# Kernel optimization log

Measured on AMD Instinct MI355X. Metric: run time of the kernel, lower is better.

The kernel has to match this reference:

```python
import jax, jax.numpy as jnp
import numpy as np

# static config (matches init_kwargs / chosen grid)
T, H, W = 8, 32, 32          # video token grid
WT, WH, WW = 4, 8, 8         # swin window
HEADS, HD = 16, 128
DIM = HEADS * HD             # 2048
LT = 256                     # text length
EPS = 1e-6
NT, NH, NW_ = T // WT, H // WH, W // WW
NWIN = NT * NH * NW_
WLEN = WT * WH * WW


def rmsnorm(x, g):
    # x: [..., HD], g: [HD]
    var = jnp.mean(x * x, axis=-1, keepdims=True)
    return x * jax.lax.rsqrt(var + EPS) * g


def setup_inputs() -> dict:
    key = jax.random.key(0)
    ks = jax.random.split(key, 8)
    s = 0.02
    Lv = T * H * W
    return {
        'vid': jax.random.normal(ks[0], (Lv, DIM), jnp.float32),
        'txt': jax.random.normal(ks[1], (LT, DIM), jnp.float32),
        'Wqkv_v': jax.random.normal(ks[2], (DIM, 3 * DIM), jnp.float32) * s,
        'bqkv_v': jnp.zeros((3 * DIM,), jnp.float32),
        'Wqkv_t': jax.random.normal(ks[3], (DIM, 3 * DIM), jnp.float32) * s,
        'bqkv_t': jnp.zeros((3 * DIM,), jnp.float32),
        'Wo_v': jax.random.normal(ks[4], (DIM, DIM), jnp.float32) * s,
        'bo_v': jnp.zeros((DIM,), jnp.float32),
        'Wo_t': jax.random.normal(ks[5], (DIM, DIM), jnp.float32) * s,
        'bo_t': jnp.zeros((DIM,), jnp.float32),
        'gq_v': jnp.ones((HD,), jnp.float32),
        'gk_v': jnp.ones((HD,), jnp.float32),
        'gq_t': jnp.ones((HD,), jnp.float32),
        'gk_t': jnp.ones((HD,), jnp.float32),
    }


def _forward(vid, txt, Wqkv_v, bqkv_v, Wqkv_t, bqkv_t, Wo_v, bo_v, Wo_t, bo_t,
             gq_v, gk_v, gq_t, gk_t):
    # per-modality QKV projections
    vqkv = vid @ Wqkv_v + bqkv_v                      # [Lv, 3*DIM]
    tqkv = txt @ Wqkv_t + bqkv_t                      # [LT, 3*DIM]
    # swin window partition: [T,H,W,C] -> [nWin, WLEN, 3, h, d]
    x = vqkv.reshape(NT, WT, NH, WH, NW_, WW, 3 * DIM)
    x = x.transpose(0, 2, 4, 1, 3, 5, 6).reshape(NWIN, WLEN, 3, HEADS, HD)
    vq, vk, vv = x[:, :, 0], x[:, :, 1], x[:, :, 2]
    t = tqkv.reshape(LT, 3, HEADS, HD)
    tq, tk, tv = t[:, 0], t[:, 1], t[:, 2]
    # QK norm (per-head RMSNorm with affine)
    vq, vk = rmsnorm(vq, gq_v), rmsnorm(vk, gk_v)
    tq, tk = rmsnorm(tq, gq_t), rmsnorm(tk, gk_t)
    # concat full text to every window (repeat_concat_idx)
    bt = lambda a: jnp.broadcast_to(a[None], (NWIN,) + a.shape)
    q = jnp.concatenate([vq, bt(tq)], axis=1)          # [nWin, S, h, d]
    k = jnp.concatenate([vk, bt(tk)], axis=1)
    v = jnp.concatenate([vv, bt(tv)], axis=1)
    # attention within each window (flash-varlen equivalent, equal lengths)
    scale = 1.0 / np.sqrt(HD).astype(np.float32)
    scores = jnp.einsum('nqhd,nkhd->nhqk', q, k) * scale
    p = jax.nn.softmax(scores, axis=-1)
    o = jnp.einsum('nhqk,nkhd->nqhd', p, v)            # [nWin, S, h, d]
    vo = o[:, :WLEN].reshape(NWIN, WLEN, DIM)
    to = o[:, WLEN:].mean(axis=0).reshape(LT, DIM)     # un-repeat text: mean over windows
    # window reverse -> flat [Lv, DIM]
    vo = vo.reshape(NT, NH, NW_, WT, WH, WW, DIM)
    vo = vo.transpose(0, 3, 1, 4, 2, 5, 6).reshape(T * H * W, DIM)
    return (vo @ Wo_v + bo_v, to @ Wo_t + bo_t)


def reference(vid, txt, Wqkv_v, bqkv_v, Wqkv_t, bqkv_t, Wo_v, bo_v, Wo_t, bo_t,
              gq_v, gk_v, gq_t, gk_t):
    return _forward(vid, txt, Wqkv_v, bqkv_v, Wqkv_t, bqkv_t, Wo_v, bo_v,
                    Wo_t, bo_t, gq_v, gk_v, gq_t, gk_t)
```

## Files before the change

kernel.cpp:

```cpp
#include <hip/hip_runtime.h>

typedef unsigned short u16;
typedef unsigned int   u32;
typedef __attribute__((ext_vector_type(8))) short short8;
typedef __attribute__((ext_vector_type(4))) float f32x4;

__device__ __forceinline__ u16 f2bf(float f) {
  union { float f; u32 u; } v; v.f = f;
  u32 r = v.u + 0x7fffu + ((v.u >> 16) & 1u);
  return (u16)(r >> 16);
}
__device__ __forceinline__ float bf2f(u32 bits) {
  union { u32 u; float f; } v; v.u = bits << 16; return v.f;
}
__device__ __forceinline__ void gl_lds16(const u16* g, u16* l) {
  __builtin_amdgcn_global_load_lds(
      (const __attribute__((address_space(1))) void*)g,
      (__attribute__((address_space(3))) void*)l, 16, 0, 0);
}

static constexpr int DIM  = 2048;
static constexpr int NQKV = 6144;

__global__ __launch_bounds__(256) void conv_f32_bf16(const float* __restrict__ in,
                                                     u16* __restrict__ out, int n4) {
  int id = blockIdx.x * 256 + threadIdx.x;
  if (id >= n4) return;
  float4 v = ((const float4*)in)[id];
  u32 lo = (u32)f2bf(v.x) | ((u32)f2bf(v.y) << 16);
  u32 hi = (u32)f2bf(v.z) | ((u32)f2bf(v.w) << 16);
  ((uint2*)out)[id] = make_uint2(lo, hi);
}

__global__ void tconv_kernel(const float* __restrict__ W, u16* __restrict__ Wt, int K, int N) {
  __shared__ float t[32][33];
  int tx = threadIdx.x, ty = threadIdx.y;
  int n0 = blockIdx.x * 32, k0 = blockIdx.y * 32;
  #pragma unroll
  for (int i = 0; i < 4; ++i)
    t[ty + i*8][tx] = W[(size_t)(k0 + ty + i*8) * N + n0 + tx];
  __syncthreads();
  #pragma unroll
  for (int i = 0; i < 4; ++i)
    Wt[(size_t)(n0 + ty + i*8) * K + k0 + tx] = f2bf(t[tx][ty + i*8]);
}

__global__ __launch_bounds__(256) void rms_kernel(u16* __restrict__ x,
                                                  const float* __restrict__ g, int nrows) {
  int w = threadIdx.x >> 6, lane = threadIdx.x & 63;
  int rid = blockIdx.x * 4 + w;
  if (rid >= nrows) return;
  u32* row = (u32*)x + (size_t)rid * 64;
  u32 u = row[lane];
  float f0 = bf2f(u & 0xffffu), f1 = bf2f(u >> 16);
  float s = f0*f0 + f1*f1;
  #pragma unroll
  for (int off = 1; off <= 32; off <<= 1) s += __shfl_xor(s, off);
  float r = rsqrtf(s * (1.0f/128.0f) + 1e-6f);
  float g0 = g[lane*2], g1 = g[lane*2+1];
  row[lane] = (u32)f2bf(f0*r*g0) | ((u32)f2bf(f1*r*g1) << 16);
}

__global__ __launch_bounds__(256)
void vtrans_kernel(const u16* __restrict__ src, u16* __restrict__ dst) {
  __shared__ u16 t[64][130];
  int nh = blockIdx.x, k0 = blockIdx.y * 64;
  const u16* s = src + ((size_t)nh*256 + k0)*128;
  u16* d = dst + (size_t)nh*128*256 + k0;
  int tid = threadIdx.x;
  #pragma unroll
  for (int it = 0; it < 4; ++it) {
    int c = tid + it*256;
    int row = c >> 4, ch = c & 15;
    short8 v = *(const short8*)(s + row*128 + ch*8);
    u32* dst32 = (u32*)&t[row][ch*8];
    const u32* v32 = (const u32*)&v;
    dst32[0] = v32[0]; dst32[1] = v32[1]; dst32[2] = v32[2]; dst32[3] = v32[3];
  }
  __syncthreads();
  #pragma unroll
  for (int it = 0; it < 4; ++it) {
    int c = tid + it*256;
    int dr = c >> 3, kg = c & 7;
    short8 v;
    #pragma unroll
    for (int j = 0; j < 8; ++j) v[j] = (short)t[kg*8+j][dr];
    *(short8*)(d + (size_t)dr*256 + kg*8) = v;
  }
}

template<int EPI>
__global__ __launch_bounds__(512, 2)
void gemm256(const u16* __restrict__ A, const u16* __restrict__ Bt,
             const float* __restrict__ bias,
             u16* __restrict__ o0, u16* __restrict__ o1, u16* __restrict__ o2,
             float* __restrict__ of, int ldo, int M, int N, int K)
{
  __shared__ __align__(16) u16 As[4][256*32];
  __shared__ __align__(16) u16 Bs[4][256*32];
  const int NT = K >> 5;
  int tid = threadIdx.x, lane = tid & 63, w = tid >> 6;
  int l15 = lane & 15, l4 = lane >> 4;
  int wm = w >> 2, wn = w & 3;

  int nbx = gridDim.x;
  int nwg = nbx * gridDim.y;
  int bid = blockIdx.y * nbx + blockIdx.x;
  int cpx = nwg >> 3;
  int swz = (bid & 7) * cpx + (bid >> 3);
  int n0 = (swz % nbx) * 256, m0 = (swz / nbx) * 256;

  int srow = tid >> 2, skc = (tid & 3) ^ ((tid >> 3) & 3);
  const u16* aS = A  + (size_t)(m0 + srow) * K + skc * 8;
  const u16* bS = Bt + (size_t)(n0 + srow) * K + skc * 8;
  const size_t halfStride = 128 * (size_t)K;
  const int ldsBase = w * 512;

  #define STAGE_A(slot, tt, half) \
    gl_lds16(aS + (size_t)(tt)*32 + (half)*halfStride, &As[slot][(half)*4096 + ldsBase])
  #define STAGE_B(slot, tt, half) \
    gl_lds16(bS + (size_t)(tt)*32 + (half)*halfStride, &Bs[slot][(half)*4096 + ldsBase])

  #pragma unroll
  for (int pt = 0; pt < 3; ++pt) {
    STAGE_A(pt, pt, 0); STAGE_A(pt, pt, 1);
    STAGE_B(pt, pt, 0); STAGE_B(pt, pt, 1);
  }

  f32x4 acc[8][4] = {};

  for (int t = 0; t < NT; ++t) {
    if (t < NT - 2)       asm volatile("s_waitcnt vmcnt(8)" ::: "memory");
    else if (t == NT - 2) asm volatile("s_waitcnt vmcnt(4)" ::: "memory");
    else                  asm volatile("s_waitcnt vmcnt(0)" ::: "memory");
    __builtin_amdgcn_s_barrier();
    asm volatile("" ::: "memory");

    const u16* ab = As[t & 3];
    const u16* bb = Bs[t & 3];
    bool st = (t + 3 < NT);
    int slot = (t + 3) & 3;

    short8 bf_[4];
    #pragma unroll
    for (int j = 0; j < 4; ++j) {
      int rb = wn*64 + j*16 + l15;
      bf_[j] = *(const short8*)((const char*)bb + rb*64 + ((l4 ^ ((rb>>1)&3))*16));
    }

    short8 af[4];
    #pragma unroll
    for (int i = 0; i < 4; ++i) {
      int ra = wm*128 + i*16 + l15;
      af[i] = *(const short8*)((const char*)ab + ra*64 + ((l4 ^ ((ra>>1)&3))*16));
    }
    if (st) { STAGE_A(slot, t+3, 0); STAGE_A(slot, t+3, 1); }
    __builtin_amdgcn_s_setprio(1);
    #pragma unroll
    for (int i = 0; i < 4; ++i)
      #pragma unroll
      for (int j = 0; j < 4; ++j)
        acc[i][j] = __builtin_amdgcn_mfma_f32_16x16x32_bf16(af[i], bf_[j], acc[i][j], 0, 0, 0);
    __builtin_amdgcn_s_setprio(0);

    #pragma unroll
    for (int i = 0; i < 4; ++i) {
      int ra = wm*128 + 64 + i*16 + l15;
      af[i] = *(const short8*)((const char*)ab + ra*64 + ((l4 ^ ((ra>>1)&3))*16));
    }
    if (st) { STAGE_B(slot, t+3, 0); STAGE_B(slot, t+3, 1); }
    __builtin_amdgcn_s_setprio(1);
    #pragma unroll
    for (int i = 0; i < 4; ++i)
      #pragma unroll
      for (int j = 0; j < 4; ++j)
        acc[4+i][j] = __builtin_amdgcn_mfma_f32_16x16x32_bf16(af[i], bf_[j], acc[4+i][j], 0, 0, 0);
    __builtin_amdgcn_s_setprio(0);
  }
  #undef STAGE_A
  #undef STAGE_B

  #pragma unroll
  for (int i = 0; i < 8; ++i)
    #pragma unroll
    for (int j = 0; j < 4; ++j)
      #pragma unroll
      for (int r = 0; r < 4; ++r) {
        int m = m0 + wm*128 + i*16 + l4*4 + r;
        int n = n0 + wn*64  + j*16 + l15;
        float v = acc[i][j][r] + bias[n];
        if (EPI == 0) {
          int which = n >> 11, head = (n >> 7) & 15, d = n & 127;
          int t = m >> 10, hh = (m >> 5) & 31, ww = m & 31;
          int win = ((t>>2)<<4) + ((hh>>3)<<2) + (ww>>3);
          int p   = ((t&3)<<6) + ((hh&7)<<3) + (ww&7);
          u16* dst = which == 0 ? o0 : (which == 1 ? o1 : o2);
          dst[((size_t)(win*16 + head)*256 + p)*128 + d] = f2bf(v);
        } else {
          of[(size_t)m * ldo + n] = v;
        }
      }
}

template<int EPI>
__global__ __launch_bounds__(256)
void gemm128(const u16* __restrict__ A, const u16* __restrict__ Bt,
             const float* __restrict__ bias,
             u16* __restrict__ o0, u16* __restrict__ o1, u16* __restrict__ o2,
             float* __restrict__ of, int ldo, int M, int N, int K)
{
  __shared__ __align__(16) u16 As[128*32];
  __shared__ __align__(16) u16 Bs[128*32];
  int tid = threadIdx.x, lane = tid & 63, w = tid >> 6;
  int l15 = lane & 15, l4 = lane >> 4;
  int m0 = blockIdx.y * 128, n0 = blockIdx.x * 128;
  int wr = (w >> 1) * 64, wc = (w & 1) * 64;
  f32x4 acc[4][4] = {};

  int o0b = (w    )*1024 + lane*16;
  int o1b = (w + 4)*1024 + lane*16;
  int r0 = o0b >> 6, c0 = ((o0b >> 4) & 3) ^ ((r0 >> 1) & 3);
  int r1 = o1b >> 6, c1 = ((o1b >> 4) & 3) ^ ((r1 >> 1) & 3);
  const u16* a0 = A  + (size_t)(m0 + r0)*K + c0*8;
  const u16* a1 = A  + (size_t)(m0 + r1)*K + c1*8;
  const u16* b0 = Bt + (size_t)(n0 + r0)*K + c0*8;
  const u16* b1 = Bt + (size_t)(n0 + r1)*K + c1*8;
  u16* dA0 = As + (w    )*512;
  u16* dA1 = As + (w + 4)*512;
  u16* dB0 = Bs + (w    )*512;
  u16* dB1 = Bs + (w + 4)*512;

  for (int k0 = 0; k0 < K; k0 += 32) {
    gl_lds16(a0 + k0, dA0);
    gl_lds16(a1 + k0, dA1);
    gl_lds16(b0 + k0, dB0);
    gl_lds16(b1 + k0, dB1);
    __syncthreads();
    short8 af[4], bfr[4];
    #pragma unroll
    for (int t = 0; t < 4; ++t) {
      int ra = wr + t*16 + l15;
      af[t]  = *(const short8*)((const char*)As + ra*64 + ((l4 ^ ((ra>>1)&3))*16));
      int rb = wc + t*16 + l15;
      bfr[t] = *(const short8*)((const char*)Bs + rb*64 + ((l4 ^ ((rb>>1)&3))*16));
    }
    #pragma unroll
    for (int i = 0; i < 4; ++i)
      #pragma unroll
      for (int j = 0; j < 4; ++j)
        acc[i][j] = __builtin_amdgcn_mfma_f32_16x16x32_bf16(af[i], bfr[j], acc[i][j], 0, 0, 0);
    __syncthreads();
  }

  #pragma unroll
  for (int i = 0; i < 4; ++i)
    #pragma unroll
    for (int j = 0; j < 4; ++j)
      #pragma unroll
      for (int r = 0; r < 4; ++r) {
        int m = m0 + wr + i*16 + l4*4 + r;
        int n = n0 + wc + j*16 + l15;
        float v = acc[i][j][r] + bias[n];
        if (EPI == 1) {
          int which = n >> 11, head = (n >> 7) & 15, d = n & 127;
          u16* dst = which == 0 ? o0 : (which == 1 ? o1 : o2);
          dst[((size_t)head*256 + m)*128 + d] = f2bf(v);
        } else {
          of[(size_t)m * ldo + n] = v;
        }
      }
}

__global__ __launch_bounds__(512)
void attn_kernel(const u16* __restrict__ vq, const u16* __restrict__ vk, const u16* __restrict__ vv,
                 const u16* __restrict__ tq, const u16* __restrict__ tk, const u16* __restrict__ tv,
                 const float* __restrict__ gq_v, const float* __restrict__ gq_t,
                 u16* __restrict__ vo, float* __restrict__ to_acc)
{
  __shared__ __align__(16) u16 Ks[64*128];
  __shared__ __align__(16) u16 Vt[128*64];
  __shared__ __align__(16) u16 Ps[8][16*80];
  int tid = threadIdx.x, lane = tid & 63, w = tid >> 6;
  int l15 = lane & 15, l4 = lane >> 4;
  int nh_ = blockIdx.x;
  int h = nh_ & 15;
  int n = nh_ >> 4;
  int qt = blockIdx.y * 128 + w * 16;

  const u16* Qb; const float* gq;
  if (qt < 256) { Qb = vq + ((size_t)nh_*256 + qt)*128; gq = gq_v; }
  else          { Qb = tq + ((size_t)h  *256 + (qt-256))*128; gq = gq_t; }
  short8 qf[4];
  float qv[4][8];
  float ss = 0.f;
  #pragma unroll
  for (int dt = 0; dt < 4; ++dt) {
    qf[dt] = *(const short8*)(Qb + l15*128 + l4*8 + dt*32);
    #pragma unroll
    for (int j = 0; j < 8; ++j) {
      float f = bf2f((u16)qf[dt][j]);
      qv[dt][j] = f; ss += f*f;
    }
  }
  ss += __shfl_xor(ss, 16); ss += __shfl_xor(ss, 32);
  float rr = rsqrtf(ss * (1.0f/128.0f) + 1e-6f);
  #pragma unroll
  for (int dt = 0; dt < 4; ++dt) {
    float4 g0 = *(const float4*)(gq + l4*8 + dt*32);
    float4 g1 = *(const float4*)(gq + l4*8 + dt*32 + 4);
    qf[dt][0] = (short)f2bf(qv[dt][0]*rr*g0.x); qf[dt][1] = (short)f2bf(qv[dt][1]*rr*g0.y);
    qf[dt][2] = (short)f2bf(qv[dt][2]*rr*g0.z); qf[dt][3] = (short)f2bf(qv[dt][3]*rr*g0.w);
    qf[dt][4] = (short)f2bf(qv[dt][4]*rr*g1.x); qf[dt][5] = (short)f2bf(qv[dt][5]*rr*g1.y);
    qf[dt][6] = (short)f2bf(qv[dt][6]*rr*g1.z); qf[dt][7] = (short)f2bf(qv[dt][7]*rr*g1.w);
  }

  int oK0 = w*1024 + lane*16, oK1 = oK0 + 8192;
  int kr0 = oK0 >> 8, kc0 = ((oK0 >> 4) & 15) ^ (kr0 & 7);
  int kr1 = oK1 >> 8, kc1 = ((oK1 >> 4) & 15) ^ (kr1 & 7);
  int vd0 = oK0 >> 7, vc0 = ((oK0 >> 4) & 7) ^ (vd0 & 7);
  int vd1 = oK1 >> 7, vc1 = ((oK1 >> 4) & 7) ^ (vd1 & 7);
  u16* KD0 = Ks + (w*1024)/2;  u16* KD1 = Ks + (w*1024 + 8192)/2;
  u16* VD0 = Vt + (w*1024)/2;  u16* VD1 = Vt + (w*1024 + 8192)/2;

  f32x4 o_[8] = {};
  float m_run[4] = {-1e30f,-1e30f,-1e30f,-1e30f};
  float l_run[4] = {0.f,0.f,0.f,0.f};
  const float scale = 0.08838834764831845f;

  for (int c = 0; c < 8; ++c) {
    int kb = c * 64;
    const u16* Kc; const u16* Vb; int vkb;
    if (kb < 256) { Kc = vk + ((size_t)nh_*256 + kb)*128; Vb = vv + (size_t)nh_*128*256; vkb = kb; }
    else          { Kc = tk + ((size_t)h  *256 + (kb-256))*128; Vb = tv + (size_t)h*128*256; vkb = kb - 256; }
    gl_lds16(Kc + kr0*128 + kc0*8, KD0);
    gl_lds16(Kc + kr1*128 + kc1*8, KD1);
    gl_lds16(Vb + (size_t)vd0*256 + vkb + vc0*8, VD0);
    gl_lds16(Vb + (size_t)vd1*256 + vkb + vc1*8, VD1);
    __syncthreads();

    f32x4 s4[4];
    #pragma unroll
    for (int kt = 0; kt < 4; ++kt) {
      f32x4 sa = {0.f,0.f,0.f,0.f};
      int key = kt*16 + l15;
      #pragma unroll
      for (int dt = 0; dt < 4; ++dt) {
        int c16b = l4 + dt*4;
        short8 kf = *(const short8*)((const char*)Ks + key*256 + (((c16b ^ (key&7)))*16));
        sa = __builtin_amdgcn_mfma_f32_16x16x32_bf16(qf[dt], kf, sa, 0, 0, 0);
      }
      s4[kt] = sa;
    }

    float f_[4];
    #pragma unroll
    for (int r = 0; r < 4; ++r) {
      float mx = fmaxf(fmaxf(s4[0][r], s4[1][r]), fmaxf(s4[2][r], s4[3][r])) * scale;
      #pragma unroll
      for (int off = 1; off <= 8; off <<= 1) mx = fmaxf(mx, __shfl_xor(mx, off));
      float nm = fmaxf(m_run[r], mx);
      f_[r] = __expf(m_run[r] - nm);
      m_run[r] = nm;
    }
    float p[4][4];
    #pragma unroll
    for (int kt = 0; kt < 4; ++kt)
      #pragma unroll
      for (int r = 0; r < 4; ++r)
        p[kt][r] = __expf(s4[kt][r]*scale - m_run[r]);
    #pragma unroll
    for (int r = 0; r < 4; ++r) {
      float sum = p[0][r] + p[1][r] + p[2][r] + p[3][r];
      #pragma unroll
      for (int off = 1; off <= 8; off <<= 1) sum += __shfl_xor(sum, off);
      l_run[r] = l_run[r]*f_[r] + sum;
    }
    #pragma unroll
    for (int dt = 0; dt < 8; ++dt) {
      f32x4 t = o_[dt];
      t[0]*=f_[0]; t[1]*=f_[1]; t[2]*=f_[2]; t[3]*=f_[3];
      o_[dt] = t;
    }

    u16* pb = Ps[w];
    #pragma unroll
    for (int kt = 0; kt < 4; ++kt)
      #pragma unroll
      for (int r = 0; r < 4; ++r)
        pb[(l4*4 + r)*80 + kt*16 + l15] = f2bf(p[kt][r]);
    __syncthreads();
    #pragma unroll
    for (int ks = 0; ks < 2; ++ks) {
      short8 pa = *(const short8*)((const char*)pb + l15*160 + ks*64 + l4*16);
      #pragma unroll
      for (int dt = 0; dt < 8; ++dt) {
        int d = dt*16 + l15;
        short8 vf = *(const short8*)((const char*)Vt + d*128 + (((ks*4 + l4) ^ (d&7))<<4));
        o_[dt] = __builtin_amdgcn_mfma_f32_16x16x32_bf16(pa, vf, o_[dt], 0, 0, 0);
      }
    }
    __syncthreads();
  }

  float inv[4];
  #pragma unroll
  for (int r = 0; r < 4; ++r) inv[r] = 1.0f / l_run[r];
  int nt = n >> 4, nh2 = (n >> 2) & 3, nw = n & 3;
  #pragma unroll
  for (int dt = 0; dt < 8; ++dt) {
    int d = dt*16 + l15;
    int col = h*128 + d;
    #pragma unroll
    for (int r = 0; r < 4; ++r) {
      float val = o_[dt][r] * inv[r];
      int q = qt + l4*4 + r;
      if (q < 256) {
        int wt = q >> 6, wh = (q >> 3) & 7, ww = q & 7;
        int rg = ((nt*4 + wt)*32 + (nh2*8 + wh))*32 + (nw*8 + ww);
        vo[(size_t)rg*2048 + col] = f2bf(val);
      } else {
        atomicAdd(to_acc + (size_t)(q - 256)*2048 + col, val * (1.0f/32.0f));
      }
    }
  }
}

extern "C" void kernel_launch(void* const* d_in, const int* in_sizes, int n_in,
                              void* d_out, int out_size, void* d_ws, size_t ws_size,
                              hipStream_t stream) {
  const float* vid    = (const float*)d_in[0];
  const float* txt    = (const float*)d_in[1];
  const float* Wqkv_v = (const float*)d_in[2];
  const float* bqkv_v = (const float*)d_in[3];
  const float* Wqkv_t = (const float*)d_in[4];
  const float* bqkv_t = (const float*)d_in[5];
  const float* Wo_v   = (const float*)d_in[6];
  const float* bo_v   = (const float*)d_in[7];
  const float* Wo_t   = (const float*)d_in[8];
  const float* bo_t   = (const float*)d_in[9];
  const float* gq_v   = (const float*)d_in[10];
  const float* gk_v   = (const float*)d_in[11];
  const float* gq_t   = (const float*)d_in[12];
  const float* gk_t   = (const float*)d_in[13];
  float* out = (float*)d_out;

  char* p = (char*)d_ws;
  u16* vid_bf   = (u16*)p;  p += 8192ull*2048*2;
  u16* txt_bf   = (u16*)p;  p += 256ull*2048*2;
  u16* Wqkv_v_t = (u16*)p;  p += 6144ull*2048*2;
  u16* Wqkv_t_t = (u16*)p;  p += 6144ull*2048*2;
  u16* Wo_v_t   = (u16*)p;  p += 2048ull*2048*2;
  u16* Wo_t_t   = (u16*)p;  p += 2048ull*2048*2;
  u16* vq_w     = (u16*)p;  p += 32ull*16*256*128*2;
  u16* vk_w     = (u16*)p;  p += 32ull*16*256*128*2;
  u16* vv_w     = (u16*)p;  p += 32ull*16*256*128*2;
  u16* tq_w     = (u16*)p;  p += 16ull*256*128*2;
  u16* tk_w     = (u16*)p;  p += 16ull*256*128*2;
  u16* tv_w     = (u16*)p;  p += 16ull*256*128*2;
  u16* vo_pre   = (u16*)p;  p += 8192ull*2048*2;
  float* to_pre = (float*)p; p += 256ull*2048*4;
  u16* to_bf    = (u16*)p;  p += 256ull*2048*2;
  u16* vvT = vid_bf;
  u16* tvT = vid_bf + 512ull*128*256;

  hipMemsetAsync(to_pre, 0, 256ull*2048*4, stream);

  conv_f32_bf16<<<dim3(16384), dim3(256), 0, stream>>>(vid, vid_bf, 8192*2048/4);
  conv_f32_bf16<<<dim3(512),   dim3(256), 0, stream>>>(txt, txt_bf, 256*2048/4);
  tconv_kernel<<<dim3(192,64), dim3(32,8), 0, stream>>>(Wqkv_v, Wqkv_v_t, 2048, 6144);
  tconv_kernel<<<dim3(192,64), dim3(32,8), 0, stream>>>(Wqkv_t, Wqkv_t_t, 2048, 6144);
  tconv_kernel<<<dim3(64,64),  dim3(32,8), 0, stream>>>(Wo_v,   Wo_v_t,   2048, 2048);
  tconv_kernel<<<dim3(64,64),  dim3(32,8), 0, stream>>>(Wo_t,   Wo_t_t,   2048, 2048);

  gemm256<0><<<dim3(24,32), dim3(512), 0, stream>>>(vid_bf, Wqkv_v_t, bqkv_v,
      vq_w, vk_w, vv_w, nullptr, 0, 8192, NQKV, DIM);
  gemm128<1><<<dim3(48,2),  dim3(256), 0, stream>>>(txt_bf, Wqkv_t_t, bqkv_t,
      tq_w, tk_w, tv_w, nullptr, 0, 256, NQKV, DIM);

  vtrans_kernel<<<dim3(512,4), dim3(256), 0, stream>>>(vv_w, vvT);
  vtrans_kernel<<<dim3(16,4),  dim3(256), 0, stream>>>(tv_w, tvT);

  rms_kernel<<<dim3(32768), dim3(256), 0, stream>>>(vk_w, gk_v, 32*16*256);
  rms_kernel<<<dim3(1024),  dim3(256), 0, stream>>>(tk_w, gk_t, 16*256);

  attn_kernel<<<dim3(512,4), dim3(512), 0, stream>>>(vq_w, vk_w, vvT, tq_w, tk_w, tvT,
                                                     gq_v, gq_t, vo_pre, to_pre);

  conv_f32_bf16<<<dim3(512), dim3(256), 0, stream>>>(to_pre, to_bf, 256*2048/4);

  gemm256<2><<<dim3(8,32), dim3(512), 0, stream>>>(vo_pre, Wo_v_t, bo_v,
      nullptr, nullptr, nullptr, out, 2048, 8192, 2048, 2048);
  gemm128<2><<<dim3(16,2), dim3(256), 0, stream>>>(to_bf, Wo_t_t, bo_t,
      nullptr, nullptr, nullptr, out + 16777216, 2048, 256, 2048, 2048);
}
```

Before: 641.8 us.

## Double-buffer K/V in attention, process 32 queries per wave, remap grid

The attention kernel now has each wave handle two 16-row query tiles, so one block covers 256 queries and the grid halves to 1024 blocks. The intent is to reuse each K/V tile loaded into LDS across twice as many queries. K/V tiles are double-buffered so the next chunk's global-to-LDS load overlaps the current chunk's compute, which also removes one barrier per iteration. It adds s_setprio around the MFMA sections and swizzles the block index so blocks sharing an XCD are grouped. The cost is twice the LDS for K/V plus more registers for two accumulator sets, which may lower occupancy.

```diff
diff --git a/kernel.cpp b/kernel.cpp
--- a/kernel.cpp
+++ b/kernel.cpp
@@ -277,41 +277,52 @@
                  const float* __restrict__ gq_v, const float* __restrict__ gq_t,
                  u16* __restrict__ vo, float* __restrict__ to_acc)
 {
-  __shared__ __align__(16) u16 Ks[64*128];
-  __shared__ __align__(16) u16 Vt[128*64];
-  __shared__ __align__(16) u16 Ps[8][16*80];
+  __shared__ __align__(16) u16 Ks[2*64*128];
+  __shared__ __align__(16) u16 Vt[2*128*64];
+  __shared__ __align__(16) u16 Ps[8][32*88];
   int tid = threadIdx.x, lane = tid & 63, w = tid >> 6;
   int l15 = lane & 15, l4 = lane >> 4;
-  int nh_ = blockIdx.x;
+  int bid = blockIdx.x;
+  int logical = (bid & 7) * 128 + (bid >> 3);
+  int nh_ = logical >> 1, y = logical & 1;
   int h = nh_ & 15;
   int n = nh_ >> 4;
-  int qt = blockIdx.y * 128 + w * 16;
 
   const u16* Qb; const float* gq;
-  if (qt < 256) { Qb = vq + ((size_t)nh_*256 + qt)*128; gq = gq_v; }
-  else          { Qb = tq + ((size_t)h  *256 + (qt-256))*128; gq = gq_t; }
-  short8 qf[4];
-  float qv[4][8];
-  float ss = 0.f;
-  #pragma unroll
-  for (int dt = 0; dt < 4; ++dt) {
-    qf[dt] = *(const short8*)(Qb + l15*128 + l4*8 + dt*32);
-    #pragma unroll
-    for (int j = 0; j < 8; ++j) {
-      float f = bf2f((u16)qf[dt][j]);
-      qv[dt][j] = f; ss += f*f;
-    }
-  }
-  ss += __shfl_xor(ss, 16); ss += __shfl_xor(ss, 32);
-  float rr = rsqrtf(ss * (1.0f/128.0f) + 1e-6f);
+  if (y == 0) { Qb = vq + ((size_t)nh_*256 + w*32)*128; gq = gq_v; }
+  else        { Qb = tq + ((size_t)h  *256 + w*32)*128; gq = gq_t; }
+  float g0v[4][4], g1v[4][4];
   #pragma unroll
   for (int dt = 0; dt < 4; ++dt) {
     float4 g0 = *(const float4*)(gq + l4*8 + dt*32);
     float4 g1 = *(const float4*)(gq + l4*8 + dt*32 + 4);
-    qf[dt][0] = (short)f2bf(qv[dt][0]*rr*g0.x); qf[dt][1] = (short)f2bf(qv[dt][1]*rr*g0.y);
-    qf[dt][2] = (short)f2bf(qv[dt][2]*rr*g0.z); qf[dt][3] = (short)f2bf(qv[dt][3]*rr*g0.w);
-    qf[dt][4] = (short)f2bf(qv[dt][4]*rr*g1.x); qf[dt][5] = (short)f2bf(qv[dt][5]*rr*g1.y);
-    qf[dt][6] = (short)f2bf(qv[dt][6]*rr*g1.z); qf[dt][7] = (short)f2bf(qv[dt][7]*rr*g1.w);
+    g0v[dt][0]=g0.x; g0v[dt][1]=g0.y; g0v[dt][2]=g0.z; g0v[dt][3]=g0.w;
+    g1v[dt][0]=g1.x; g1v[dt][1]=g1.y; g1v[dt][2]=g1.z; g1v[dt][3]=g1.w;
+  }
+  short8 qf[2][4];
+  #pragma unroll
+  for (int qi = 0; qi < 2; ++qi) {
+    float qv[4][8];
+    float ss = 0.f;
+    #pragma unroll
+    for (int dt = 0; dt < 4; ++dt) {
+      qf[qi][dt] = *(const short8*)(Qb + (size_t)(qi*16 + l15)*128 + l4*8 + dt*32);
+      #pragma unroll
+      for (int j = 0; j < 8; ++j) {
+        float f = bf2f((u16)qf[qi][dt][j]);
+        qv[dt][j] = f; ss += f*f;
+      }
+    }
+    ss += __shfl_xor(ss, 16); ss += __shfl_xor(ss, 32);
+    float rr = rsqrtf(ss * (1.0f/128.0f) + 1e-6f);
+    #pragma unroll
+    for (int dt = 0; dt < 4; ++dt) {
+      #pragma unroll
+      for (int j = 0; j < 4; ++j) {
+        qf[qi][dt][j]   = (short)f2bf(qv[dt][j]  *rr*g0v[dt][j]);
+        qf[qi][dt][4+j] = (short)f2bf(qv[dt][4+j]*rr*g1v[dt][j]);
+      }
+    }
   }
 
   int oK0 = w*1024 + lane*16, oK1 = oK0 + 8192;
@@ -319,107 +330,131 @@
   int kr1 = oK1 >> 8, kc1 = ((oK1 >> 4) & 15) ^ (kr1 & 7);
   int vd0 = oK0 >> 7, vc0 = ((oK0 >> 4) & 7) ^ (vd0 & 7);
   int vd1 = oK1 >> 7, vc1 = ((oK1 >> 4) & 7) ^ (vd1 & 7);
-  u16* KD0 = Ks + (w*1024)/2;  u16* KD1 = Ks + (w*1024 + 8192)/2;
-  u16* VD0 = Vt + (w*1024)/2;  u16* VD1 = Vt + (w*1024 + 8192)/2;
-
-  f32x4 o_[8] = {};
-  float m_run[4] = {-1e30f,-1e30f,-1e30f,-1e30f};
-  float l_run[4] = {0.f,0.f,0.f,0.f};
+
+  f32x4 o_[2][8] = {};
+  float m_run[2][4] = {{-1e30f,-1e30f,-1e30f,-1e30f},{-1e30f,-1e30f,-1e30f,-1e30f}};
+  float l_run[2][4] = {};
   const float scale = 0.08838834764831845f;
+  u16* pb = Ps[w];
+
+  {
+    const u16* Kc = vk + (size_t)nh_*256*128;
+    const u16* Vb = vv + (size_t)nh_*128*256;
+    gl_lds16(Kc + kr0*128 + kc0*8, Ks + w*512);
+    gl_lds16(Kc + kr1*128 + kc1*8, Ks + w*512 + 4096);
+    gl_lds16(Vb + (size_t)vd0*256 + vc0*8, Vt + w*512);
+    gl_lds16(Vb + (size_t)vd1*256 + vc1*8, Vt + w*512 + 4096);
+  }
+  __syncthreads();
 
   for (int c = 0; c < 8; ++c) {
-    int kb = c * 64;
-    const u16* Kc; const u16* Vb; int vkb;
-    if (kb < 256) { Kc = vk + ((size_t)nh_*256 + kb)*128; Vb = vv + (size_t)nh_*128*256; vkb = kb; }
-    else          { Kc = tk + ((size_t)h  *256 + (kb-256))*128; Vb = tv + (size_t)h*128*256; vkb = kb - 256; }
-    gl_lds16(Kc + kr0*128 + kc0*8, KD0);
-    gl_lds16(Kc + kr1*128 + kc1*8, KD1);
-    gl_lds16(Vb + (size_t)vd0*256 + vkb + vc0*8, VD0);
-    gl_lds16(Vb + (size_t)vd1*256 + vkb + vc1*8, VD1);
-    __syncthreads();
-
-    f32x4 s4[4];
-    #pragma unroll
-    for (int kt = 0; kt < 4; ++kt) {
-      f32x4 sa = {0.f,0.f,0.f,0.f};
-      int key = kt*16 + l15;
-      #pragma unroll
-      for (int dt = 0; dt < 4; ++dt) {
-        int c16b = l4 + dt*4;
-        short8 kf = *(const short8*)((const char*)Ks + key*256 + (((c16b ^ (key&7)))*16));
-        sa = __builtin_amdgcn_mfma_f32_16x16x32_bf16(qf[dt], kf, sa, 0, 0, 0);
-      }
-      s4[kt] = sa;
-    }
-
-    float f_[4];
-    #pragma unroll
-    for (int r = 0; r < 4; ++r) {
-      float mx = fmaxf(fmaxf(s4[0][r], s4[1][r]), fmaxf(s4[2][r], s4[3][r])) * scale;
-      #pragma unroll
-      for (int off = 1; off <= 8; off <<= 1) mx = fmaxf(mx, __shfl_xor(mx, off));
-      float nm = fmaxf(m_run[r], mx);
-      f_[r] = __expf(m_run[r] - nm);
-      m_run[r] = nm;
-    }
-    float p[4][4];
-    #pragma unroll
-    for (int kt = 0; kt < 4; ++kt)
-      #pragma unroll
-      for (int r = 0; r < 4; ++r)
-        p[kt][r] = __expf(s4[kt][r]*scale - m_run[r]);
-    #pragma unroll
-    for (int r = 0; r < 4; ++r) {
-      float sum = p[0][r] + p[1][r] + p[2][r] + p[3][r];
-      #pragma unroll
-      for (int off = 1; off <= 8; off <<= 1) sum += __shfl_xor(sum, off);
-      l_run[r] = l_run[r]*f_[r] + sum;
-    }
-    #pragma unroll
-    for (int dt = 0; dt < 8; ++dt) {
-      f32x4 t = o_[dt];
-      t[0]*=f_[0]; t[1]*=f_[1]; t[2]*=f_[2]; t[3]*=f_[3];
-      o_[dt] = t;
-    }
-
-    u16* pb = Ps[w];
-    #pragma unroll
-    for (int kt = 0; kt < 4; ++kt)
-      #pragma unroll
-      for (int r = 0; r < 4; ++r)
-        pb[(l4*4 + r)*80 + kt*16 + l15] = f2bf(p[kt][r]);
-    __syncthreads();
+    int b = c & 1;
+    if (c < 7) {
+      int kb = (c + 1) * 64;
+      const u16* Kc; const u16* Vb; int vkb;
+      if (kb < 256) { Kc = vk + ((size_t)nh_*256 + kb)*128; Vb = vv + (size_t)nh_*128*256; vkb = kb; }
+      else          { Kc = tk + ((size_t)h  *256 + (kb-256))*128; Vb = tv + (size_t)h*128*256; vkb = kb - 256; }
+      int b2 = b ^ 1;
+      gl_lds16(Kc + kr0*128 + kc0*8, Ks + b2*8192 + w*512);
+      gl_lds16(Kc + kr1*128 + kc1*8, Ks + b2*8192 + w*512 + 4096);
+      gl_lds16(Vb + (size_t)vd0*256 + vkb + vc0*8, Vt + b2*8192 + w*512);
+      gl_lds16(Vb + (size_t)vd1*256 + vkb + vc1*8, Vt + b2*8192 + w*512 + 4096);
+    }
+    const char* KsB = (const char*)(Ks + b*8192);
+    const char* VtB = (const char*)(Vt + b*8192);
+
+    #pragma unroll
+    for (int qi = 0; qi < 2; ++qi) {
+      f32x4 s4[4];
+      __builtin_amdgcn_s_setprio(1);
+      #pragma unroll
+      for (int kt = 0; kt < 4; ++kt) {
+        int key = kt*16 + l15;
+        f32x4 sa = {0.f,0.f,0.f,0.f};
+        #pragma unroll
+        for (int dt = 0; dt < 4; ++dt) {
+          int c16b = l4 + dt*4;
+          short8 kf = *(const short8*)(KsB + key*256 + ((c16b ^ (key&7))*16));
+          sa = __builtin_amdgcn_mfma_f32_16x16x32_bf16(qf[qi][dt], kf, sa, 0, 0, 0);
+        }
+        s4[kt] = sa;
+      }
+      __builtin_amdgcn_s_setprio(0);
+
+      float f_[4];
+      #pragma unroll
+      for (int r = 0; r < 4; ++r) {
+        float mx = fmaxf(fmaxf(s4[0][r], s4[1][r]), fmaxf(s4[2][r], s4[3][r])) * scale;
+        #pragma unroll
+        for (int off = 1; off <= 8; off <<= 1) mx = fmaxf(mx, __shfl_xor(mx, off));
+        float nm = fmaxf(m_run[qi][r], mx);
+        f_[r] = __expf(m_run[qi][r] - nm);
+        m_run[qi][r] = nm;
+      }
+      float p[4][4];
+      #pragma unroll
+      for (int kt = 0; kt < 4; ++kt)
+        #pragma unroll
+        for (int r = 0; r < 4; ++r)
+          p[kt][r] = __expf(s4[kt][r]*scale - m_run[qi][r]);
+      #pragma unroll
+      for (int r = 0; r < 4; ++r) {
+        float sum = p[0][r] + p[1][r] + p[2][r] + p[3][r];
+        #pragma unroll
+        for (int off = 1; off <= 8; off <<= 1) sum += __shfl_xor(sum, off);
+        l_run[qi][r] = l_run[qi][r]*f_[r] + sum;
+      }
+      #pragma unroll
+      for (int dt = 0; dt < 8; ++dt) {
+        f32x4 t = o_[qi][dt];
+        t[0]*=f_[0]; t[1]*=f_[1]; t[2]*=f_[2]; t[3]*=f_[3];
+        o_[qi][dt] = t;
+      }
+      #pragma unroll
+      for (int kt = 0; kt < 4; ++kt)
+        #pragma unroll
+        for (int r = 0; r < 4; ++r)
+          pb[(qi*16 + l4*4 + r)*88 + kt*16 + l15] = f2bf(p[kt][r]);
+    }
+
     #pragma unroll
     for (int ks = 0; ks < 2; ++ks) {
-      short8 pa = *(const short8*)((const char*)pb + l15*160 + ks*64 + l4*16);
+      short8 pa0 = *(const short8*)((const char*)pb + (l15     )*176 + ks*64 + l4*16);
+      short8 pa1 = *(const short8*)((const char*)pb + (16 + l15)*176 + ks*64 + l4*16);
+      __builtin_amdgcn_s_setprio(1);
       #pragma unroll
       for (int dt = 0; dt < 8; ++dt) {
         int d = dt*16 + l15;
-        short8 vf = *(const short8*)((const char*)Vt + d*128 + (((ks*4 + l4) ^ (d&7))<<4));
-        o_[dt] = __builtin_amdgcn_mfma_f32_16x16x32_bf16(pa, vf, o_[dt], 0, 0, 0);
-      }
+        short8 vf = *(const short8*)(VtB + d*128 + (((ks*4 + l4) ^ (d&7))<<4));
+        o_[0][dt] = __builtin_amdgcn_mfma_f32_16x16x32_bf16(pa0, vf, o_[0][dt], 0, 0, 0);
+        o_[1][dt] = __builtin_amdgcn_mfma_f32_16x16x32_bf16(pa1, vf, o_[1][dt], 0, 0, 0);
+      }
+      __builtin_amdgcn_s_setprio(0);
     }
     __syncthreads();
   }
 
-  float inv[4];
-  #pragma unroll
-  for (int r = 0; r < 4; ++r) inv[r] = 1.0f / l_run[r];
   int nt = n >> 4, nh2 = (n >> 2) & 3, nw = n & 3;
   #pragma unroll
-  for (int dt = 0; dt < 8; ++dt) {
-    int d = dt*16 + l15;
-    int col = h*128 + d;
-    #pragma unroll
-    for (int r = 0; r < 4; ++r) {
-      float val = o_[dt][r] * inv[r];
-      int q = qt + l4*4 + r;
-      if (q < 256) {
-        int wt = q >> 6, wh = (q >> 3) & 7, ww = q & 7;
-        int rg = ((nt*4 + wt)*32 + (nh2*8 + wh))*32 + (nw*8 + ww);
-        vo[(size_t)rg*2048 + col] = f2bf(val);
-      } else {
-        atomicAdd(to_acc + (size_t)(q - 256)*2048 + col, val * (1.0f/32.0f));
+  for (int qi = 0; qi < 2; ++qi) {
+    float inv[4];
+    #pragma unroll
+    for (int r = 0; r < 4; ++r) inv[r] = 1.0f / l_run[qi][r];
+    #pragma unroll
+    for (int dt = 0; dt < 8; ++dt) {
+      int d = dt*16 + l15;
+      int col = h*128 + d;
+      #pragma unroll
+      for (int r = 0; r < 4; ++r) {
+        float val = o_[qi][dt][r] * inv[r];
+        int qrow = w*32 + qi*16 + l4*4 + r;
+        if (y == 0) {
+          int wt = qrow >> 6, wh = (qrow >> 3) & 7, ww = qrow & 7;
+          int rg = ((nt*4 + wt)*32 + (nh2*8 + wh))*32 + (nw*8 + ww);
+          vo[(size_t)rg*2048 + col] = f2bf(val);
+        } else {
+          atomicAdd(to_acc + (size_t)qrow*2048 + col, val * (1.0f/32.0f));
+        }
       }
     }
   }
@@ -483,8 +518,8 @@
   rms_kernel<<<dim3(32768), dim3(256), 0, stream>>>(vk_w, gk_v, 32*16*256);
   rms_kernel<<<dim3(1024),  dim3(256), 0, stream>>>(tk_w, gk_t, 16*256);
 
-  attn_kernel<<<dim3(512,4), dim3(512), 0, stream>>>(vq_w, vk_w, vvT, tq_w, tk_w, tvT,
-                                                     gq_v, gq_t, vo_pre, to_pre);
+  attn_kernel<<<dim3(1024), dim3(512), 0, stream>>>(vq_w, vk_w, vvT, tq_w, tk_w, tvT,
+                                                    gq_v, gq_t, vo_pre, to_pre);
 
   conv_f32_bf16<<<dim3(512), dim3(256), 0, stream>>>(to_pre, to_bf, 256*2048/4);
 
```

Measured after the change: 661.6 us. 1.03x slower.
